# Optimization experiments

Measured on AMD Instinct MI355X. Metric: run time of the kernel, lower is better.

## Reference

```python
import jax, jax.numpy as jnp
import numpy as np

B, NF, S, L, H, MID, KS, NC, DENSE = 16, 8, 16, 256, 128, 32, 8, 10, 512
COEFF = 0.1
BN_EPS = 1e-5


def _normalize(x):
    return x / jnp.maximum(jnp.linalg.norm(x, axis=-1, keepdims=True), 1e-12)


def _sparsemax(z):
    # sparsemax over last axis (Martins & Astudillo 2016)
    zs = jnp.flip(jnp.sort(z, axis=-1), axis=-1)
    k = jnp.arange(1, z.shape[-1] + 1, dtype=z.dtype)
    cum = jnp.cumsum(zs, axis=-1)
    support = (1.0 + k * zs) > cum
    ksup = jnp.sum(support, axis=-1, keepdims=True)
    tau = (jnp.take_along_axis(cum, ksup - 1, axis=-1) - 1.0) / ksup.astype(z.dtype)
    return jnp.maximum(z - tau, 0.0)


def _bn_ncl(x, g, b, m, v):  # eval-mode BatchNorm1d on [N, C, L]
    return g[None, :, None] * (x - m[None, :, None]) * jax.lax.rsqrt(v[None, :, None] + BN_EPS) + b[None, :, None]


def _bn_nc(x, g, b, m, v):  # eval-mode BatchNorm1d on [N, C]
    return g * (x - m) * jax.lax.rsqrt(v + BN_EPS) + b


def _conv(x, w, pad):
    return jax.lax.conv_general_dilated(x, w, (1,), [(pad, pad)], dimension_numbers=('NCH', 'OIH', 'NCH'))


def _maxpool2(x):  # MaxPool1d(kernel=2, stride=2, padding=1): -inf padded
    return jax.lax.reduce_window(x, -jnp.inf, jax.lax.max, (1, 1, 2), (1, 1, 2), ((0, 0), (0, 0), (1, 1)))


def _cnn(x, cw1, bn1, cw2, bn2, cw3, bn3):
    x = _maxpool2(jax.nn.relu(_bn_ncl(_conv(x, cw1, KS // 2), *bn1)))
    x = _maxpool2(jax.nn.relu(_bn_ncl(_conv(x, cw2, 4), *bn2)))
    x = _maxpool2(jax.nn.relu(_bn_ncl(_conv(x, cw3, 4), *bn3)))
    return jnp.mean(x, axis=-1)  # AdaptiveAvgPool1d(1) -> [N, H]


def _alpha_beta(x, cw1, bn1, cw2, bn2, cw3, bn3, Wq, bq, Wk, bk, Wv, bv):
    b = x.shape[0]
    xf = jnp.transpose(x, (1, 0, 2, 3)).reshape(NF, b * S, 1, L)
    rep = jax.vmap(_cnn)(xf, cw1, bn1, cw2, bn2, cw3, bn3)  # [F, B*S, H]
    rep = rep.reshape(NF, b, S, H)
    Q = jax.nn.elu(rep @ Wq + bq)
    K = jax.nn.leaky_relu(rep @ Wk + bk)
    V = jax.nn.leaky_relu(rep @ Wv + bv)
    # mean_t(Q @ K^T) == Q @ mean_t(K); then scale by sqrt(d_k)
    scores = jnp.einsum('fbsh,fbh->fbs', Q, jnp.mean(K, axis=2)) / jnp.sqrt(jnp.float32(H))
    intra_aw = _sparsemax(scores)                             # [F, B, S]
    Z = _normalize(jnp.einsum('fbs,fbsh->fbh', intra_aw, V))  # [F, B, H]
    Kn = _normalize(rep)
    inter_scores = jnp.einsum('ibh,fbsh->ifbs', Z, Kn)        # cosine scores (Z already unit-norm)
    inter_aw = _sparsemax(inter_scores)                       # [I, F, B, S]
    U = jnp.einsum('ifbs,fbsh->ibh', inter_aw, rep) / NF      # mean over feature axis f
    Hc = _normalize(jnp.concatenate([Z, U], axis=-1))         # [F, B, 2H]
    feat = jnp.transpose(Hc, (1, 0, 2)).reshape(b, NF * 2 * H)
    return feat, intra_aw, inter_aw


def _forward(src_x, src_y, tgt_x, cw1, bn1_g, bn1_b, bn1_m, bn1_v, cw2, bn2_g, bn2_b, bn2_m, bn2_v, cw3, bn3_g, bn3_b, bn3_m, bn3_v, Wq, bq, Wk, bk, Wv, bv, bnc1_g, bnc1_b, bnc1_m, bnc1_v, W1, b1, bnc2_g, bnc2_b, bnc2_m, bnc2_v, W2, b2):
    bn1 = (bn1_g, bn1_b, bn1_m, bn1_v)
    bn2 = (bn2_g, bn2_b, bn2_m, bn2_v)
    bn3 = (bn3_g, bn3_b, bn3_m, bn3_v)
    sf, sa, sb = _alpha_beta(src_x, cw1, bn1, cw2, bn2, cw3, bn3, Wq, bq, Wk, bk, Wv, bv)
    _, ta, tb = _alpha_beta(tgt_x, cw1, bn1, cw2, bn2, cw3, bn3, Wq, bq, Wk, bk, Wv, bv)
    h = _bn_nc(sf, bnc1_g, bnc1_b, bnc1_m, bnc1_v) @ W1 + b1
    h = jax.nn.leaky_relu(_bn_nc(h, bnc2_g, bnc2_b, bnc2_m, bnc2_v))
    y_pred = jax.nn.softmax(h @ W2 + b2, axis=-1)
    # MMD domain losses (detached in original via torch.tensor(list))
    da = jnp.mean(sa - ta, axis=-2)                           # [F, S]
    loss_a = COEFF * jnp.mean(jnp.linalg.norm(da, axis=-1))
    db = jnp.mean(sb - tb, axis=-2)                           # [I, F, S]
    loss_b = COEFF * jnp.mean(jnp.sqrt(jnp.sum(db * db, axis=(1, 2))))
    dom = jax.lax.stop_gradient(loss_a + loss_b)
    # CrossEntropyLoss applied to already-softmaxed preds, as in source
    logp = jax.nn.log_softmax(y_pred, axis=-1)
    ce = -jnp.mean(logp[jnp.arange(y_pred.shape[0]), src_y])
    return y_pred, ce + dom


def setup_inputs() -> dict:
    ks = jax.random.split(jax.random.key(0), 40)
    rn = lambda i, sh, s=1.0: s * jax.random.normal(ks[i], sh, dtype=jnp.float32)
    ru = lambda i, sh, lo, hi: jax.random.uniform(ks[i], sh, jnp.float32, lo, hi)
    return {
        'src_x': rn(0, (B, NF, S, L)),
        'src_y': jax.random.randint(ks[1], (B,), 0, NC),
        'tgt_x': rn(2, (B, NF, S, L)),
        'cw1': rn(3, (NF, MID, 1, KS), 0.1),
        'bn1_g': ru(4, (NF, MID), 0.75, 1.25), 'bn1_b': rn(5, (NF, MID), 0.1),
        'bn1_m': rn(6, (NF, MID), 0.1), 'bn1_v': ru(7, (NF, MID), 0.5, 1.5),
        'cw2': rn(8, (NF, 2 * MID, MID, 8), 0.05),
        'bn2_g': ru(9, (NF, 2 * MID), 0.75, 1.25), 'bn2_b': rn(10, (NF, 2 * MID), 0.1),
        'bn2_m': rn(11, (NF, 2 * MID), 0.1), 'bn2_v': ru(12, (NF, 2 * MID), 0.5, 1.5),
        'cw3': rn(13, (NF, H, 2 * MID, 8), 0.05),
        'bn3_g': ru(14, (NF, H), 0.75, 1.25), 'bn3_b': rn(15, (NF, H), 0.1),
        'bn3_m': rn(16, (NF, H), 0.1), 'bn3_v': ru(17, (NF, H), 0.5, 1.5),
        'Wq': rn(18, (H, H), 0.05), 'bq': rn(19, (H,), 0.02),
        'Wk': rn(20, (H, H), 0.05), 'bk': rn(21, (H,), 0.02),
        'Wv': rn(22, (H, H), 0.05), 'bv': rn(23, (H,), 0.02),
        'bnc1_g': ru(24, (NF * 2 * H,), 0.75, 1.25), 'bnc1_b': rn(25, (NF * 2 * H,), 0.1),
        'bnc1_m': rn(26, (NF * 2 * H,), 0.1), 'bnc1_v': ru(27, (NF * 2 * H,), 0.5, 1.5),
        'W1': rn(28, (NF * 2 * H, DENSE), 0.03), 'b1': rn(29, (DENSE,), 0.02),
        'bnc2_g': ru(30, (DENSE,), 0.75, 1.25), 'bnc2_b': rn(31, (DENSE,), 0.1),
        'bnc2_m': rn(32, (DENSE,), 0.1), 'bnc2_v': ru(33, (DENSE,), 0.5, 1.5),
        'W2': rn(34, (DENSE, NC), 0.05), 'b2': rn(35, (NC,), 0.02),
    }


def reference(src_x, src_y, tgt_x, cw1, bn1_g, bn1_b, bn1_m, bn1_v, cw2, bn2_g, bn2_b, bn2_m, bn2_v, cw3, bn3_g, bn3_b, bn3_m, bn3_v, Wq, bq, Wk, bk, Wv, bv, bnc1_g, bnc1_b, bnc1_m, bnc1_v, W1, b1, bnc2_g, bnc2_b, bnc2_m, bnc2_v, W2, b2):
    return _forward(src_x, src_y, tgt_x, cw1, bn1_g, bn1_b, bn1_m, bn1_v, cw2, bn2_g, bn2_b, bn2_m, bn2_v, cw3, bn3_g, bn3_b, bn3_m, bn3_v, Wq, bq, Wk, bk, Wv, bv, bnc1_g, bnc1_b, bnc1_m, bnc1_v, W1, b1, bnc2_g, bnc2_b, bnc2_m, bnc2_v, W2, b2)
```

## Files before the change

### kernel.cpp

```cpp
#include <hip/hip_runtime.h>

typedef unsigned short u16;
typedef unsigned int u32;
typedef __attribute__((ext_vector_type(8))) short bfrag;
typedef __attribute__((ext_vector_type(4))) float ffrag;
typedef __attribute__((ext_vector_type(16))) float ffrag16;

__device__ __forceinline__ float lrelu(float x) { return x >= 0.f ? x : 0.01f * x; }
__device__ __forceinline__ float eluf(float x)  { return x > 0.f ? x : expm1f(x); }
__device__ __forceinline__ u16 f2bf(float f) {
    u32 x = __float_as_uint(f);
    return (u16)((x + 0x7fffu + ((x >> 16) & 1u)) >> 16);
}
__device__ __forceinline__ u16 f2bt(float f) {
    return (u16)(__float_as_uint(f) >> 16);
}
__device__ __forceinline__ float bf2f(u16 u) {
    return __uint_as_float(((u32)u) << 16);
}

__device__ void sparsemax16(const float* z, float* out) {
    float zs[16];
    for (int i = 0; i < 16; ++i) zs[i] = z[i];
    for (int i = 1; i < 16; ++i) {
        float key = zs[i]; int j = i - 1;
        while (j >= 0 && zs[j] < key) { zs[j + 1] = zs[j]; --j; }
        zs[j + 1] = key;
    }
    float cum[16];
    cum[0] = zs[0];
    for (int i = 1; i < 16; ++i) cum[i] = cum[i - 1] + zs[i];
    int ksup = 0;
    for (int k = 1; k <= 16; ++k)
        if (1.0f + (float)k * zs[k - 1] > cum[k - 1]) ksup++;
    if (ksup < 1) ksup = 1;
    float tau = (cum[ksup - 1] - 1.0f) / (float)ksup;
    for (int i = 0; i < 16; ++i) out[i] = fmaxf(z[i] - tau, 0.0f);
}

__global__ __launch_bounds__(256) void k_wprep(
    const float* __restrict__ w2, const float* __restrict__ w3,
    const float* __restrict__ Wq, const float* __restrict__ Wk,
    const float* __restrict__ Wv,
    u16* __restrict__ wpk2, u16* __restrict__ wpk3, u16* __restrict__ wqkv)
{
    int s0 = (blockIdx.x * 256 + threadIdx.x) * 4;
    if (s0 < 131072) {
        float4 v = *reinterpret_cast<const float4*>(w2 + s0);
        float vv[4] = {v.x, v.y, v.z, v.w};
#pragma unroll
        for (int t = 0; t < 4; ++t) {
            int s = s0 + t;
            int kc = s & 7, ci = (s >> 3) & 31, co = (s >> 8) & 63, f = s >> 14;
            int L = ((ci >> 3) << 4) | (co & 15);
            wpk2[f * 16384 + (co >> 4) * 4096 + kc * 512 + L * 8 + (ci & 7)] = f2bf(vv[t]);
        }
    } else if (s0 < 131072 + 524288) {
        int s0b = s0 - 131072;
        float4 v = *reinterpret_cast<const float4*>(w3 + s0b);
        float vv[4] = {v.x, v.y, v.z, v.w};
#pragma unroll
        for (int t = 0; t < 4; ++t) {
            int s = s0b + t;
            int tap = s & 7, ci = (s >> 3) & 63, co = (s >> 9) & 127, f = s >> 16;
            int kt = tap * 4 + (ci >> 4);
            int L = (((ci >> 3) & 1) << 5) | (co & 31);
            wpk3[f * 65536 + (co >> 5) * 16384 + kt * 512 + L * 8 + (ci & 7)] = f2bf(vv[t]);
        }
    } else if (s0 < 131072 + 524288 + 49152) {
        int s0c = s0 - 655360;
        int proj = s0c >> 14, sidx0 = s0c & 16383;
        const float* W = proj == 0 ? Wq : (proj == 1 ? Wk : Wv);
        float4 v = *reinterpret_cast<const float4*>(W + sidx0);
        float vv[4] = {v.x, v.y, v.z, v.w};
#pragma unroll
        for (int t = 0; t < 4; ++t) {
            int s = sidx0 + t;
            int n = s & 127, k = s >> 7;
            int r = k & 31;
            int L = ((r >> 3) << 4) | (n & 15);
            wqkv[proj * 16384 + (n >> 4) * 2048 + (k >> 5) * 512 + L * 8 + (r & 7)] = f2bf(vv[t]);
        }
    }
}

#define S1T_STRIDE 40
#define S2T_STRIDE 72
#define RB2_STRIDE 68
#define RB3_STRIDE 140
#define RB_OFF 6336
#define SMEM_U16 (RB_OFF + 67 * RB3_STRIDE)

__global__ __launch_bounds__(256, 3) void k_cnn(
    const float* __restrict__ xs, const float* __restrict__ xt,
    const float* __restrict__ w1, const float* __restrict__ g1, const float* __restrict__ b1,
    const float* __restrict__ m1, const float* __restrict__ v1,
    const float* __restrict__ g2, const float* __restrict__ b2,
    const float* __restrict__ m2, const float* __restrict__ v2,
    const float* __restrict__ g3, const float* __restrict__ b3,
    const float* __restrict__ m3, const float* __restrict__ v3,
    const u16* __restrict__ wpk2, const u16* __restrict__ wpk3,
    float* __restrict__ rep)
{
    __shared__ __align__(16) u16 smem[SMEM_U16];
    float* xin = (float*)(smem + RB_OFF);

    int tid = threadIdx.x, blk = blockIdx.x;
    int pass = blk >> 11, f = (blk >> 8) & 7, n = blk & 255;
    int bb = n >> 4, ss = n & 15;
    int lane = tid & 63, w = tid >> 6;
    const float* x = pass ? xt : xs;
    float* rep_p = rep + (size_t)pass * 262144;

    {
        u32* z = (u32*)smem;
        for (int i = tid; i < 80; i += 256) z[i] = 0;
        for (int i = tid; i < 360; i += 256) z[2660 + i] = 0;
        if (tid < 4) { xin[tid] = 0.f; xin[260 + tid] = 0.f; }
        const float* xr = x + (((size_t)bb * 8 + f) * 16 + ss) * 256;
        for (int i = tid; i < 256; i += 256) xin[i + 4] = xr[i];
    }
    __syncthreads();

    if (tid < 208) {
        int cc = tid & 7, jc = tid >> 3;
        int co0 = cc * 4, j0 = jc * 5;
        float wr[4][8];
        for (int c = 0; c < 4; ++c) {
            const float4* q = reinterpret_cast<const float4*>(w1 + ((size_t)f * 32 + co0 + c) * 8);
            float4 a = q[0], bq = q[1];
            wr[c][0] = a.x; wr[c][1] = a.y; wr[c][2] = a.z; wr[c][3] = a.w;
            wr[c][4] = bq.x; wr[c][5] = bq.y; wr[c][6] = bq.z; wr[c][7] = bq.w;
        }
        int px[10];
        for (int i = 0; i < 10; ++i) {
            int p = 2 * j0 - 1 + i;
            px[i] = p < 0 ? 0 : (p > 256 ? 256 : p);
        }
        float acc[4][10];
        for (int c = 0; c < 4; ++c) for (int i = 0; i < 10; ++i) acc[c][i] = 0.f;
        for (int k = 0; k < 8; ++k) {
            float xv[10];
            for (int i = 0; i < 10; ++i) xv[i] = xin[px[i] + k];
            for (int c = 0; c < 4; ++c)
                for (int i = 0; i < 10; ++i) acc[c][i] += wr[c][k] * xv[i];
        }
        float scv[4], shv[4];
        for (int c = 0; c < 4; ++c) {
            int co = co0 + c;
            scv[c] = g1[f * 32 + co] * rsqrtf(v1[f * 32 + co] + 1e-5f);
            shv[c] = b1[f * 32 + co] - m1[f * 32 + co] * scv[c];
        }
        for (int jj = 0; jj < 5; ++jj) {
            int j = j0 + jj;
            if (j < 129) {
                ushort4 pk;
                {
                    float a0 = fmaxf(acc[0][2*jj] * scv[0] + shv[0], 0.f);
                    float a1 = fmaxf(acc[0][2*jj+1] * scv[0] + shv[0], 0.f);
                    pk.x = f2bt(fmaxf(a0, a1));
                }
                {
                    float a0 = fmaxf(acc[1][2*jj] * scv[1] + shv[1], 0.f);
                    float a1 = fmaxf(acc[1][2*jj+1] * scv[1] + shv[1], 0.f);
                    pk.y = f2bt(fmaxf(a0, a1));
                }
                {
                    float a0 = fmaxf(acc[2][2*jj] * scv[2] + shv[2], 0.f);
                    float a1 = fmaxf(acc[2][2*jj+1] * scv[2] + shv[2], 0.f);
                    pk.z = f2bt(fmaxf(a0, a1));
                }
                {
                    float a0 = fmaxf(acc[3][2*jj] * scv[3] + shv[3], 0.f);
                    float a1 = fmaxf(acc[3][2*jj+1] * scv[3] + shv[3], 0.f);
                    pk.w = f2bt(fmaxf(a0, a1));
                }
                *reinterpret_cast<ushort4*>(&smem[(j + 4) * S1T_STRIDE + co0]) = pk;
            }
        }
    }
    __syncthreads();

    {
        bfrag B2[2][8];
        {
            const bfrag* gB = reinterpret_cast<const bfrag*>(wpk2);
            int wN = w & 1;
#pragma unroll
            for (int t = 0; t < 2; ++t)
#pragma unroll
                for (int kc = 0; kc < 8; ++kc)
                    B2[t][kc] = gB[(((size_t)f * 4 + (wN * 2 + t)) * 8 + kc) * 64 + lane];
        }
        int wM = w >> 1, wN = w & 1;
        float sc2[2], sh2[2];
        int co2[2];
#pragma unroll
        for (int t = 0; t < 2; ++t) {
            int co = (wN * 2 + t) * 16 + (lane & 15);
            co2[t] = co;
            sc2[t] = g2[f * 64 + co] * rsqrtf(v2[f * 64 + co] + 1e-5f);
            sh2[t] = b2[f * 64 + co] - m2[f * 64 + co] * sc2[t];
        }
        int arow = lane & 15, ci0 = (lane >> 4) << 3;
        int mtlo = wM ? 5 : 0, mthi = wM ? 9 : 5;
        for (int mt = mtlo; mt < mthi; ++mt) {
            ffrag C0 = {0.f, 0.f, 0.f, 0.f}, C1 = {0.f, 0.f, 0.f, 0.f};
            int rb = mt * 16 + arow;
#pragma unroll
            for (int kc = 0; kc < 8; ++kc) {
                bfrag A = *reinterpret_cast<const bfrag*>(&smem[(rb + kc) * S1T_STRIDE + ci0]);
                C0 = __builtin_amdgcn_mfma_f32_16x16x32_bf16(A, B2[0][kc], C0, 0, 0, 0);
                C1 = __builtin_amdgcn_mfma_f32_16x16x32_bf16(A, B2[1][kc], C1, 0, 0, 0);
            }
            int p0 = mt * 16 + ((lane >> 4) << 2);
#pragma unroll
            for (int r = 0; r < 4; ++r) {
                int p = p0 + r;
                if (p < 130) {
                    smem[RB_OFF + p * RB2_STRIDE + co2[0]] = f2bt(fmaxf(C0[r] * sc2[0] + sh2[0], 0.f));
                    smem[RB_OFF + p * RB2_STRIDE + co2[1]] = f2bt(fmaxf(C1[r] * sc2[1] + sh2[1], 0.f));
                }
            }
        }
    }
    __syncthreads();

    {
        u32* z = (u32*)smem;
        for (int i = tid; i < 144; i += 256) z[i] = 0;
        for (int i = tid; i < 612; i += 256) z[2520 + i] = 0;
    }
    {
        const u32* rb2 = reinterpret_cast<const u32*>(smem + RB_OFF);
        u32* s2 = reinterpret_cast<u32*>(smem);
        for (int e = tid; e < 66 * 32; e += 256) {
            int j = e >> 5, c2 = e & 31;
            u32 v;
            if (j == 0) {
                v = rb2[c2];
            } else if (j == 65) {
                v = rb2[129 * 34 + c2];
            } else {
                u32 a = rb2[(2 * j - 1) * 34 + c2];
                u32 b = rb2[(2 * j) * 34 + c2];
                float a0 = bf2f((u16)a), a1 = bf2f((u16)(a >> 16));
                float b0 = bf2f((u16)b), b1 = bf2f((u16)(b >> 16));
                u16 m0 = a0 > b0 ? (u16)a : (u16)b;
                u16 m1 = a1 > b1 ? (u16)(a >> 16) : (u16)(b >> 16);
                v = (u32)m0 | ((u32)m1 << 16);
            }
            s2[(j + 4) * 36 + c2] = v;
        }
    }
    __syncthreads();

    {
        int am = lane & 31, hk = (lane >> 5) << 3;
        const bfrag* gB3 = reinterpret_cast<const bfrag*>(wpk3);
        size_t bbase = (((size_t)f * 4 + w) * 32) * 64 + lane;
        ffrag16 C0 = {0.f,0.f,0.f,0.f,0.f,0.f,0.f,0.f,0.f,0.f,0.f,0.f,0.f,0.f,0.f,0.f};
        ffrag16 C1 = {0.f,0.f,0.f,0.f,0.f,0.f,0.f,0.f,0.f,0.f,0.f,0.f,0.f,0.f,0.f,0.f};
        ffrag16 C2 = {0.f,0.f,0.f,0.f,0.f,0.f,0.f,0.f,0.f,0.f,0.f,0.f,0.f,0.f,0.f,0.f};
#pragma unroll 4
        for (int kt = 0; kt < 32; ++kt) {
            int row0 = am + (kt >> 2);
            int ci0 = (kt & 3) * 16 + hk;
            bfrag B = gB3[bbase + (size_t)kt * 64];
            bfrag A0 = *reinterpret_cast<const bfrag*>(&smem[row0 * S2T_STRIDE + ci0]);
            bfrag A1 = *reinterpret_cast<const bfrag*>(&smem[(row0 + 32) * S2T_STRIDE + ci0]);
            bfrag A2 = *reinterpret_cast<const bfrag*>(&smem[(row0 + 64) * S2T_STRIDE + ci0]);
            C0 = __builtin_amdgcn_mfma_f32_32x32x16_bf16(A0, B, C0, 0, 0, 0);
            C1 = __builtin_amdgcn_mfma_f32_32x32x16_bf16(A1, B, C1, 0, 0, 0);
            C2 = __builtin_amdgcn_mfma_f32_32x32x16_bf16(A2, B, C2, 0, 0, 0);
        }
        int ncol = w * 32 + am;
        float sc = g3[f * 128 + ncol] * rsqrtf(v3[f * 128 + ncol] + 1e-5f);
        float sh = b3[f * 128 + ncol] - m3[f * 128 + ncol] * sc;
        int prow_off = (lane >> 5) << 2;
#pragma unroll
        for (int reg = 0; reg < 16; ++reg) {
            int pr = (reg & 3) + 8 * (reg >> 2) + prow_off;
            smem[RB_OFF + pr * RB3_STRIDE + ncol] = f2bt(fmaxf(C0[reg] * sc + sh, 0.f));
            smem[RB_OFF + (32 + pr) * RB3_STRIDE + ncol] = f2bt(fmaxf(C1[reg] * sc + sh, 0.f));
            int p2 = 64 + pr;
            if (p2 < 67)
                smem[RB_OFF + p2 * RB3_STRIDE + ncol] = f2bt(fmaxf(C2[reg] * sc + sh, 0.f));
        }
    }
    __syncthreads();

    if (tid < 128) {
        int co = tid;
        float sum = bf2f(smem[RB_OFF + 0 * RB3_STRIDE + co]);
        for (int j = 1; j < 34; ++j) {
            float a0 = bf2f(smem[RB_OFF + (2 * j - 1) * RB3_STRIDE + co]);
            float a1 = bf2f(smem[RB_OFF + (2 * j) * RB3_STRIDE + co]);
            sum += fmaxf(a0, a1);
        }
        rep_p[(((size_t)f * 256) + n) * 128 + co] = sum * (1.0f / 34.0f);
    }
}

__global__ __launch_bounds__(256) void k_attn1(
    const float* __restrict__ rep, const u16* __restrict__ wqkv,
    const float* __restrict__ bq, const float* __restrict__ bk,
    const float* __restrict__ bv,
    float* __restrict__ Zn, float* __restrict__ rninv, float* __restrict__ iaw)
{
    __shared__ __align__(16) u16 repbf[16 * 136];
    __shared__ float KmL[128], ZL[128], awL[16], scoresL[16], r2L[16];
    __shared__ float spart[4][4][4];
    __shared__ float redL[4];
    int tid = threadIdx.x;
    int pass = blockIdx.x >> 7, f = (blockIdx.x >> 4) & 7, b = blockIdx.x & 15;
    const float* rp = rep + (size_t)pass * 262144 + ((size_t)f * 256 + b * 16) * 128;
    float* Zn_p = Zn + (size_t)pass * 16384;
    float* rninv_p = rninv + (size_t)pass * 2048;
    float* iaw_p = iaw + (size_t)pass * 2048;

    {
        int s = tid >> 4, i = tid & 15, h0 = i * 8;
        const float4* q4 = reinterpret_cast<const float4*>(rp + s * 128 + h0);
        float4 a = q4[0], c = q4[1];
        float p2 = a.x*a.x + a.y*a.y + a.z*a.z + a.w*a.w
                 + c.x*c.x + c.y*c.y + c.z*c.z + c.w*c.w;
        bfrag pk;
        pk[0] = (short)f2bt(a.x); pk[1] = (short)f2bt(a.y);
        pk[2] = (short)f2bt(a.z); pk[3] = (short)f2bt(a.w);
        pk[4] = (short)f2bt(c.x); pk[5] = (short)f2bt(c.y);
        pk[6] = (short)f2bt(c.z); pk[7] = (short)f2bt(c.w);
        *reinterpret_cast<bfrag*>(&repbf[s * 136 + h0]) = pk;
        p2 += __shfl_xor(p2, 1); p2 += __shfl_xor(p2, 2);
        p2 += __shfl_xor(p2, 4); p2 += __shfl_xor(p2, 8);
        if (i == 0) r2L[s] = p2;
    }
    __syncthreads();

    int lane = tid & 63, w = tid >> 6, arow = lane & 15, q = lane >> 4;
    bfrag A[4];
    for (int kc = 0; kc < 4; ++kc)
        A[kc] = *reinterpret_cast<const bfrag*>(&repbf[arow * 136 + kc * 32 + q * 8]);

    float qv[2][4], vvv[2][4];
    int colv[2];
    const bfrag* BB = reinterpret_cast<const bfrag*>(wqkv);
    for (int t = 0; t < 2; ++t) {
        int nt = w * 2 + t;
        ffrag cq = {0.f,0.f,0.f,0.f}, ck = {0.f,0.f,0.f,0.f}, cv = {0.f,0.f,0.f,0.f};
        for (int kc = 0; kc < 4; ++kc) {
            int fi = (nt * 4 + kc) * 64 + lane;
            bfrag Bq = BB[fi];
            bfrag Bk = BB[2048 + fi];
            bfrag Bv = BB[4096 + fi];
            cq = __builtin_amdgcn_mfma_f32_16x16x32_bf16(A[kc], Bq, cq, 0, 0, 0);
            ck = __builtin_amdgcn_mfma_f32_16x16x32_bf16(A[kc], Bk, ck, 0, 0, 0);
            cv = __builtin_amdgcn_mfma_f32_16x16x32_bf16(A[kc], Bv, cv, 0, 0, 0);
        }
        int col = nt * 16 + arow;
        colv[t] = col;
        float bqc = bq[col], bkc = bk[col], bvc = bv[col];
        float kpt = 0.f;
        for (int r = 0; r < 4; ++r) {
            qv[t][r] = eluf(cq[r] + bqc);
            vvv[t][r] = lrelu(cv[r] + bvc);
            kpt += lrelu(ck[r] + bkc);
        }
        kpt += __shfl_xor(kpt, 16);
        kpt += __shfl_xor(kpt, 32);
        if (q == 0) KmL[col] = kpt * (1.f / 16.f);
    }
    __syncthreads();

    {
        float km0 = KmL[colv[0]], km1 = KmL[colv[1]];
        float ps[4];
        for (int r = 0; r < 4; ++r) {
            float v = qv[0][r] * km0 + qv[1][r] * km1;
            v += __shfl_xor(v, 1); v += __shfl_xor(v, 2);
            v += __shfl_xor(v, 4); v += __shfl_xor(v, 8);
            ps[r] = v;
        }
        if (arow == 0)
            for (int r = 0; r < 4; ++r) spart[w][q][r] = ps[r];
    }
    __syncthreads();
    if (tid < 16) {
        int qq = tid >> 2, rr = tid & 3;
        float sc = spart[0][qq][rr] + spart[1][qq][rr] + spart[2][qq][rr] + spart[3][qq][rr];
        scoresL[tid] = sc * 0.08838834764831845f;
        rninv_p[f * 256 + b * 16 + tid] = 1.f / fmaxf(sqrtf(r2L[tid]), 1e-12f);
    }
    __syncthreads();
    if (tid == 0) sparsemax16(scoresL, awL);
    __syncthreads();
    if (tid < 16) iaw_p[f * 256 + b * 16 + tid] = awL[tid];

    for (int t = 0; t < 2; ++t) {
        float zp = 0.f;
        for (int r = 0; r < 4; ++r) zp += awL[q * 4 + r] * vvv[t][r];
        zp += __shfl_xor(zp, 16);
        zp += __shfl_xor(zp, 32);
        if (q == 0) ZL[colv[t]] = zp;
    }
    __syncthreads();
    if (tid < 128) {
        float z = ZL[tid];
        float v = z * z;
        v += __shfl_xor(v, 1); v += __shfl_xor(v, 2); v += __shfl_xor(v, 4);
        v += __shfl_xor(v, 8); v += __shfl_xor(v, 16); v += __shfl_xor(v, 32);
        if (lane == 0) redL[w] = v;
    }
    __syncthreads();
    if (tid == 0) redL[2] = 1.f / fmaxf(sqrtf(redL[0] + redL[1]), 1e-12f);
    __syncthreads();
    if (tid < 128)
        Zn_p[((size_t)f * 16 + b) * 128 + tid] = ZL[tid] * redL[2];
}

__global__ __launch_bounds__(256) void k_attn2(
    const float* __restrict__ rep, const float* __restrict__ Zn,
    const float* __restrict__ rninv, float* __restrict__ ibw,
    const float* __restrict__ g, const float* __restrict__ bb,
    const float* __restrict__ mm, const float* __restrict__ vv,
    float* __restrict__ featbn)
{
    __shared__ float repL[16384];
    __shared__ float ZiL[128], scores[128], UL[128];
    __shared__ float awLf[8][16];
    __shared__ float redL[2];
    int tid = threadIdx.x, blk = blockIdx.x;
    int pass = blk >> 7, b = (blk >> 3) & 15, i = blk & 7;
    const float* rep_p = rep + (size_t)pass * 262144;

    for (int f = 0; f < 8; ++f) {
        const float4* src = reinterpret_cast<const float4*>(
            rep_p + ((size_t)f * 256 + b * 16) * 128);
        float4* dst = reinterpret_cast<float4*>(repL + f * 2048);
        for (int t = tid; t < 512; t += 256) dst[t] = src[t];
    }
    if (tid < 128) ZiL[tid] = Zn[(size_t)pass * 16384 + ((size_t)i * 16 + b) * 128 + tid];
    __syncthreads();

    if (tid < 128) {
        int f = tid >> 4, s = tid & 15;
        const float* rr = repL + tid * 128;
        float a = 0.f;
        for (int h = 0; h < 128; ++h) a += ZiL[h] * rr[h];
        scores[tid] = a * rninv[(size_t)pass * 2048 + f * 256 + b * 16 + s];
    }
    __syncthreads();
    if (tid < 8) {
        float aw[16];
        sparsemax16(&scores[tid * 16], aw);
        for (int s = 0; s < 16; ++s) awLf[tid][s] = aw[s];
    }
    __syncthreads();
    if (tid < 128) {
        int f = tid >> 4, s = tid & 15;
        ibw[(size_t)pass * 16384 + (((size_t)i * 8 + f) * 16 + b) * 16 + s] = awLf[f][s];
    }
    if (pass == 0) {
        if (tid < 128) {
            int h = tid;
            float u = 0.f;
            for (int f = 0; f < 8; ++f) {
                const float* rr = repL + f * 2048 + h;
                const float* aa = awLf[f];
                for (int s = 0; s < 16; ++s) u += aa[s] * rr[s * 128];
            }
            UL[h] = u * 0.125f;
        }
        __syncthreads();
        if (tid < 128) {
            int lane = tid & 63, w = tid >> 6;
            float v = ZiL[tid] * ZiL[tid] + UL[tid] * UL[tid];
            v += __shfl_xor(v, 1); v += __shfl_xor(v, 2); v += __shfl_xor(v, 4);
            v += __shfl_xor(v, 8); v += __shfl_xor(v, 16); v += __shfl_xor(v, 32);
            if (lane == 0) redL[w] = v;
        }
        __syncthreads();
        if (tid < 256) {
            float inv = 1.f / fmaxf(sqrtf(redL[0] + redL[1]), 1e-12f);
            int d = tid;
            int e = i * 256 + d;
            float val = (d < 128 ? ZiL[d] : UL[d - 128]) * inv;
            float scv = g[e] * rsqrtf(vv[e] + 1e-5f);
            featbn[b * 2048 + e] = (val - mm[e]) * scv + bb[e];
        }
    }
}

__global__ __launch_bounds__(256) void k_head1(
    const float* __restrict__ featbn,
    const float* __restrict__ W1, const float* __restrict__ b1,
    const float* __restrict__ g2, const float* __restrict__ bb2,
    const float* __restrict__ mm2, const float* __restrict__ vv2,
    float* __restrict__ h2ws)
{
    __shared__ float featL[2048];
    __shared__ float part[32][32];
    int tid = threadIdx.x, blk = blockIdx.x;
    int b = blk >> 4, cc = blk & 15;
    {
        const float4* src = reinterpret_cast<const float4*>(featbn + b * 2048);
        float4* dst = reinterpret_cast<float4*>(featL);
        for (int i = tid; i < 512; i += 256) dst[i] = src[i];
    }
    __syncthreads();
    int ks = tid >> 3, cg = tid & 7;
    int col0 = cc * 32 + cg * 4;
    float4 acc = {0.f, 0.f, 0.f, 0.f};
    const float* fl = featL + ks * 64;
    for (int c = 0; c < 64; ++c) {
        int k = ks * 64 + c;
        float4 wv = *reinterpret_cast<const float4*>(W1 + (size_t)k * 512 + col0);
        float fv = fl[c];
        acc.x += fv * wv.x; acc.y += fv * wv.y;
        acc.z += fv * wv.z; acc.w += fv * wv.w;
    }
    part[ks][cg * 4 + 0] = acc.x;
    part[ks][cg * 4 + 1] = acc.y;
    part[ks][cg * 4 + 2] = acc.z;
    part[ks][cg * 4 + 3] = acc.w;
    __syncthreads();
    if (tid < 32) {
        int colw = cc * 32 + tid;
        float s = b1[colw];
        for (int k2 = 0; k2 < 32; ++k2) s += part[k2][tid];
        float scv = g2[colw] * rsqrtf(vv2[colw] + 1e-5f);
        float val = (s - mm2[colw]) * scv + bb2[colw];
        h2ws[b * 512 + colw] = lrelu(val);
    }
}

__global__ __launch_bounds__(256) void k_tail(
    const float* __restrict__ h2ws,
    const float* __restrict__ W2, const float* __restrict__ b2,
    const float* __restrict__ sa, const float* __restrict__ ta,
    const float* __restrict__ sb, const float* __restrict__ tb,
    const int* __restrict__ sy, float* __restrict__ dout)
{
    __shared__ float h2L[8192];
    __shared__ float lgL[160], ypL[160];
    __shared__ float sA[8], sB[8];
    int tid = threadIdx.x;
    for (int i = tid; i < 8192; i += 256) h2L[i] = h2ws[i];
    if (tid < 8) { sA[tid] = 0.f; sB[tid] = 0.f; }
    __syncthreads();
    if (tid < 160) {
        int b = tid / 10, j = tid - b * 10;
        float a = b2[j];
        const float* h = h2L + b * 512;
        for (int c = 0; c < 512; ++c) a += h[c] * W2[c * 10 + j];
        lgL[tid] = a;
    }
    __syncthreads();
    if (tid < 16) {
        int b = tid;
        float mx = lgL[b * 10];
        for (int j = 1; j < 10; ++j) mx = fmaxf(mx, lgL[b * 10 + j]);
        float sum = 0.f, ex[10];
        for (int j = 0; j < 10; ++j) { ex[j] = expf(lgL[b * 10 + j] - mx); sum += ex[j]; }
        for (int j = 0; j < 10; ++j) {
            float p = ex[j] / sum;
            ypL[b * 10 + j] = p;
            dout[b * 10 + j] = p;
        }
    }
    __syncthreads();
    if (tid < 128) {
        int f = tid >> 4, s = tid & 15;
        float d = 0.f;
        for (int b = 0; b < 16; ++b) d += sa[f * 256 + b * 16 + s] - ta[f * 256 + b * 16 + s];
        d *= (1.f / 16.f);
        atomicAdd(&sA[f], d * d);
    }
    for (int e = tid; e < 1024; e += 256) {
        int i = e >> 7, f = (e >> 4) & 7, s = e & 15;
        float d = 0.f;
        int base = ((i * 8 + f) * 16) * 16 + s;
        for (int b = 0; b < 16; ++b) d += sb[base + b * 16] - tb[base + b * 16];
        d *= (1.f / 16.f);
        atomicAdd(&sB[i], d * d);
    }
    __syncthreads();
    if (tid == 0) {
        float la = 0.f, lb = 0.f;
        for (int f = 0; f < 8; ++f) la += sqrtf(sA[f]);
        for (int i = 0; i < 8; ++i) lb += sqrtf(sB[i]);
        la *= 0.1f / 8.f;
        lb *= 0.1f / 8.f;
        float ce = 0.f;
        for (int b = 0; b < 16; ++b) {
            const float* y = ypL + b * 10;
            float mx = y[0];
            for (int j = 1; j < 10; ++j) mx = fmaxf(mx, y[j]);
            float sum = 0.f;
            for (int j = 0; j < 10; ++j) sum += expf(y[j] - mx);
            float lse = mx + logf(sum);
            ce += lse - y[sy[b]];
        }
        ce *= (1.f / 16.f);
        dout[160] = ce + la + lb;
    }
}

extern "C" void kernel_launch(void* const* d_in, const int* in_sizes, int n_in,
                              void* d_out, int out_size, void* d_ws, size_t ws_size,
                              hipStream_t stream) {
    (void)in_sizes; (void)n_in; (void)out_size; (void)ws_size;
    const float* src_x = (const float*)d_in[0];
    const int*   src_y = (const int*)d_in[1];
    const float* tgt_x = (const float*)d_in[2];
    const float *cw1 = (const float*)d_in[3], *bn1g = (const float*)d_in[4],
                *bn1b = (const float*)d_in[5], *bn1m = (const float*)d_in[6],
                *bn1v = (const float*)d_in[7];
    const float *cw2 = (const float*)d_in[8], *bn2g = (const float*)d_in[9],
                *bn2b = (const float*)d_in[10], *bn2m = (const float*)d_in[11],
                *bn2v = (const float*)d_in[12];
    const float *cw3 = (const float*)d_in[13], *bn3g = (const float*)d_in[14],
                *bn3b = (const float*)d_in[15], *bn3m = (const float*)d_in[16],
                *bn3v = (const float*)d_in[17];
    const float *Wq = (const float*)d_in[18], *bq = (const float*)d_in[19],
                *Wk = (const float*)d_in[20], *bk = (const float*)d_in[21],
                *Wv = (const float*)d_in[22], *bv = (const float*)d_in[23];
    const float *bc1g = (const float*)d_in[24], *bc1b = (const float*)d_in[25],
                *bc1m = (const float*)d_in[26], *bc1v = (const float*)d_in[27];
    const float *W1 = (const float*)d_in[28], *b1 = (const float*)d_in[29];
    const float *bc2g = (const float*)d_in[30], *bc2b = (const float*)d_in[31],
                *bc2m = (const float*)d_in[32], *bc2v = (const float*)d_in[33];
    const float *W2 = (const float*)d_in[34], *b2 = (const float*)d_in[35];

    float* ws = (float*)d_ws;
    size_t o = 0;
    float* rep    = ws + o; o += (size_t)2 * 262144;
    float* Zn     = ws + o; o += (size_t)2 * 16384;
    float* rninv  = ws + o; o += (size_t)2 * 2048;
    float* ia     = ws + o; o += (size_t)2 * 2048;
    float* ib     = ws + o; o += (size_t)2 * 16384;
    float* featbn = ws + o; o += (size_t)16 * 2048;
    float* h2ws   = ws + o; o += (size_t)16 * 512;
    u16* wpk2 = (u16*)(ws + o); o += 65536;
    u16* wpk3 = (u16*)(ws + o); o += 262144;
    u16* wqkv = (u16*)(ws + o); o += 24576;

    k_wprep<<<688, 256, 0, stream>>>(cw2, cw3, Wq, Wk, Wv, wpk2, wpk3, wqkv);
    k_cnn<<<4096, 256, 0, stream>>>(src_x, tgt_x,
        cw1, bn1g, bn1b, bn1m, bn1v,
        bn2g, bn2b, bn2m, bn2v,
        bn3g, bn3b, bn3m, bn3v,
        wpk2, wpk3, rep);
    k_attn1<<<256, 256, 0, stream>>>(rep, wqkv, bq, bk, bv, Zn, rninv, ia);
    k_attn2<<<256, 256, 0, stream>>>(rep, Zn, rninv, ib, bc1g, bc1b, bc1m, bc1v, featbn);
    k_head1<<<256, 256, 0, stream>>>(featbn, W1, b1, bc2g, bc2b, bc2m, bc2v, h2ws);
    k_tail<<<1, 256, 0, stream>>>(h2ws, W2, b2, ia, ia + 2048, ib, ib + 16384,
                                  src_y, (float*)d_out);
}
```

Baseline: 298.6 us.

## Fuse attention, cross-attention and dense head into one per-batch kernel

Merges k_attn1, k_attn2 and k_head1 into a single k_mid kernel with one block per (pass, batch) pair, 32 blocks in total. Each block loops over the features and keeps Zn, rninv and the batch-normed features in shared memory. This removes two kernel launches and the Zn, rninv and featbn round trips through global memory. In exchange, the grid drops from 256 blocks to 32, and each pass-0 block streams the whole W1 matrix serially, which leaves most CUs idle and makes the work latency-bound.

New measurement: 597.1 us. +100.0%, slower.

```diff
diff --git a/kernel.cpp b/kernel.cpp
--- a/kernel.cpp
+++ b/kernel.cpp
@@ -302,235 +302,220 @@
     }
 }
 
-__global__ __launch_bounds__(256) void k_attn1(
+__global__ __launch_bounds__(256) void k_mid(
     const float* __restrict__ rep, const u16* __restrict__ wqkv,
     const float* __restrict__ bq, const float* __restrict__ bk,
     const float* __restrict__ bv,
-    float* __restrict__ Zn, float* __restrict__ rninv, float* __restrict__ iaw)
+    float* __restrict__ ia, float* __restrict__ ib,
+    const float* __restrict__ c1g, const float* __restrict__ c1b,
+    const float* __restrict__ c1m, const float* __restrict__ c1v,
+    const float* __restrict__ W1, const float* __restrict__ b1,
+    const float* __restrict__ c2g, const float* __restrict__ c2b,
+    const float* __restrict__ c2m, const float* __restrict__ c2v,
+    float* __restrict__ h2ws)
 {
     __shared__ __align__(16) u16 repbf[16 * 136];
     __shared__ float KmL[128], ZL[128], awL[16], scoresL[16], r2L[16];
     __shared__ float spart[4][4][4];
     __shared__ float redL[4];
-    int tid = threadIdx.x;
-    int pass = blockIdx.x >> 7, f = (blockIdx.x >> 4) & 7, b = blockIdx.x & 15;
-    const float* rp = rep + (size_t)pass * 262144 + ((size_t)f * 256 + b * 16) * 128;
-    float* Zn_p = Zn + (size_t)pass * 16384;
-    float* rninv_p = rninv + (size_t)pass * 2048;
-    float* iaw_p = iaw + (size_t)pass * 2048;
-
-    {
-        int s = tid >> 4, i = tid & 15, h0 = i * 8;
-        const float4* q4 = reinterpret_cast<const float4*>(rp + s * 128 + h0);
-        float4 a = q4[0], c = q4[1];
-        float p2 = a.x*a.x + a.y*a.y + a.z*a.z + a.w*a.w
-                 + c.x*c.x + c.y*c.y + c.z*c.z + c.w*c.w;
-        bfrag pk;
-        pk[0] = (short)f2bt(a.x); pk[1] = (short)f2bt(a.y);
-        pk[2] = (short)f2bt(a.z); pk[3] = (short)f2bt(a.w);
-        pk[4] = (short)f2bt(c.x); pk[5] = (short)f2bt(c.y);
-        pk[6] = (short)f2bt(c.z); pk[7] = (short)f2bt(c.w);
-        *reinterpret_cast<bfrag*>(&repbf[s * 136 + h0]) = pk;
-        p2 += __shfl_xor(p2, 1); p2 += __shfl_xor(p2, 2);
-        p2 += __shfl_xor(p2, 4); p2 += __shfl_xor(p2, 8);
-        if (i == 0) r2L[s] = p2;
-    }
-    __syncthreads();
-
-    int lane = tid & 63, w = tid >> 6, arow = lane & 15, q = lane >> 4;
-    bfrag A[4];
-    for (int kc = 0; kc < 4; ++kc)
-        A[kc] = *reinterpret_cast<const bfrag*>(&repbf[arow * 136 + kc * 32 + q * 8]);
-
-    float qv[2][4], vvv[2][4];
-    int colv[2];
-    const bfrag* BB = reinterpret_cast<const bfrag*>(wqkv);
-    for (int t = 0; t < 2; ++t) {
-        int nt = w * 2 + t;
-        ffrag cq = {0.f,0.f,0.f,0.f}, ck = {0.f,0.f,0.f,0.f}, cv = {0.f,0.f,0.f,0.f};
-        for (int kc = 0; kc < 4; ++kc) {
-            int fi = (nt * 4 + kc) * 64 + lane;
-            bfrag Bq = BB[fi];
-            bfrag Bk = BB[2048 + fi];
-            bfrag Bv = BB[4096 + fi];
-            cq = __builtin_amdgcn_mfma_f32_16x16x32_bf16(A[kc], Bq, cq, 0, 0, 0);
-            ck = __builtin_amdgcn_mfma_f32_16x16x32_bf16(A[kc], Bk, ck, 0, 0, 0);
-            cv = __builtin_amdgcn_mfma_f32_16x16x32_bf16(A[kc], Bv, cv, 0, 0, 0);
-        }
-        int col = nt * 16 + arow;
-        colv[t] = col;
-        float bqc = bq[col], bkc = bk[col], bvc = bv[col];
-        float kpt = 0.f;
-        for (int r = 0; r < 4; ++r) {
-            qv[t][r] = eluf(cq[r] + bqc);
-            vvv[t][r] = lrelu(cv[r] + bvc);
-            kpt += lrelu(ck[r] + bkc);
-        }
-        kpt += __shfl_xor(kpt, 16);
-        kpt += __shfl_xor(kpt, 32);
-        if (q == 0) KmL[col] = kpt * (1.f / 16.f);
-    }
-    __syncthreads();
-
-    {
-        float km0 = KmL[colv[0]], km1 = KmL[colv[1]];
-        float ps[4];
-        for (int r = 0; r < 4; ++r) {
-            float v = qv[0][r] * km0 + qv[1][r] * km1;
-            v += __shfl_xor(v, 1); v += __shfl_xor(v, 2);
-            v += __shfl_xor(v, 4); v += __shfl_xor(v, 8);
-            ps[r] = v;
-        }
-        if (arow == 0)
-            for (int r = 0; r < 4; ++r) spart[w][q][r] = ps[r];
-    }
-    __syncthreads();
-    if (tid < 16) {
-        int qq = tid >> 2, rr = tid & 3;
-        float sc = spart[0][qq][rr] + spart[1][qq][rr] + spart[2][qq][rr] + spart[3][qq][rr];
-        scoresL[tid] = sc * 0.08838834764831845f;
-        rninv_p[f * 256 + b * 16 + tid] = 1.f / fmaxf(sqrtf(r2L[tid]), 1e-12f);
-    }
-    __syncthreads();
-    if (tid == 0) sparsemax16(scoresL, awL);
-    __syncthreads();
-    if (tid < 16) iaw_p[f * 256 + b * 16 + tid] = awL[tid];
-
-    for (int t = 0; t < 2; ++t) {
-        float zp = 0.f;
-        for (int r = 0; r < 4; ++r) zp += awL[q * 4 + r] * vvv[t][r];
-        zp += __shfl_xor(zp, 16);
-        zp += __shfl_xor(zp, 32);
-        if (q == 0) ZL[colv[t]] = zp;
-    }
-    __syncthreads();
-    if (tid < 128) {
-        float z = ZL[tid];
-        float v = z * z;
-        v += __shfl_xor(v, 1); v += __shfl_xor(v, 2); v += __shfl_xor(v, 4);
-        v += __shfl_xor(v, 8); v += __shfl_xor(v, 16); v += __shfl_xor(v, 32);
-        if (lane == 0) redL[w] = v;
-    }
-    __syncthreads();
-    if (tid == 0) redL[2] = 1.f / fmaxf(sqrtf(redL[0] + redL[1]), 1e-12f);
-    __syncthreads();
-    if (tid < 128)
-        Zn_p[((size_t)f * 16 + b) * 128 + tid] = ZL[tid] * redL[2];
-}
-
-__global__ __launch_bounds__(256) void k_attn2(
-    const float* __restrict__ rep, const float* __restrict__ Zn,
-    const float* __restrict__ rninv, float* __restrict__ ibw,
-    const float* __restrict__ g, const float* __restrict__ bb,
-    const float* __restrict__ mm, const float* __restrict__ vv,
-    float* __restrict__ featbn)
-{
-    __shared__ float repL[16384];
-    __shared__ float ZiL[128], scores[128], UL[128];
+    __shared__ float ZnL[8][128];
+    __shared__ float rninvL[8][16];
+    __shared__ float scores2[128], UL[128];
     __shared__ float awLf[8][16];
-    __shared__ float redL[2];
+    __shared__ float featL[2048];
+    __shared__ float part[32][32];
+
     int tid = threadIdx.x, blk = blockIdx.x;
-    int pass = blk >> 7, b = (blk >> 3) & 15, i = blk & 7;
+    int pass = blk >> 4, b = blk & 15;
     const float* rep_p = rep + (size_t)pass * 262144;
+    float* ia_p = ia + (size_t)pass * 2048;
+    int lane = tid & 63, w = tid >> 6;
 
     for (int f = 0; f < 8; ++f) {
-        const float4* src = reinterpret_cast<const float4*>(
-            rep_p + ((size_t)f * 256 + b * 16) * 128);
-        float4* dst = reinterpret_cast<float4*>(repL + f * 2048);
-        for (int t = tid; t < 512; t += 256) dst[t] = src[t];
-    }
-    if (tid < 128) ZiL[tid] = Zn[(size_t)pass * 16384 + ((size_t)i * 16 + b) * 128 + tid];
-    __syncthreads();
-
-    if (tid < 128) {
-        int f = tid >> 4, s = tid & 15;
-        const float* rr = repL + tid * 128;
-        float a = 0.f;
-        for (int h = 0; h < 128; ++h) a += ZiL[h] * rr[h];
-        scores[tid] = a * rninv[(size_t)pass * 2048 + f * 256 + b * 16 + s];
-    }
-    __syncthreads();
-    if (tid < 8) {
-        float aw[16];
-        sparsemax16(&scores[tid * 16], aw);
-        for (int s = 0; s < 16; ++s) awLf[tid][s] = aw[s];
-    }
-    __syncthreads();
-    if (tid < 128) {
-        int f = tid >> 4, s = tid & 15;
-        ibw[(size_t)pass * 16384 + (((size_t)i * 8 + f) * 16 + b) * 16 + s] = awLf[f][s];
-    }
-    if (pass == 0) {
+        __syncthreads();
+        const float* rp = rep_p + ((size_t)f * 256 + b * 16) * 128;
+        {
+            int s = tid >> 4, i = tid & 15, h0 = i * 8;
+            const float4* q4 = reinterpret_cast<const float4*>(rp + s * 128 + h0);
+            float4 a = q4[0], c = q4[1];
+            float p2 = a.x*a.x + a.y*a.y + a.z*a.z + a.w*a.w
+                     + c.x*c.x + c.y*c.y + c.z*c.z + c.w*c.w;
+            bfrag pk;
+            pk[0] = (short)f2bt(a.x); pk[1] = (short)f2bt(a.y);
+            pk[2] = (short)f2bt(a.z); pk[3] = (short)f2bt(a.w);
+            pk[4] = (short)f2bt(c.x); pk[5] = (short)f2bt(c.y);
+            pk[6] = (short)f2bt(c.z); pk[7] = (short)f2bt(c.w);
+            *reinterpret_cast<bfrag*>(&repbf[s * 136 + h0]) = pk;
+            p2 += __shfl_xor(p2, 1); p2 += __shfl_xor(p2, 2);
+            p2 += __shfl_xor(p2, 4); p2 += __shfl_xor(p2, 8);
+            if (i == 0) r2L[s] = p2;
+        }
+        __syncthreads();
+
+        int arow = lane & 15, q = lane >> 4;
+        bfrag A[4];
+        for (int kc = 0; kc < 4; ++kc)
+            A[kc] = *reinterpret_cast<const bfrag*>(&repbf[arow * 136 + kc * 32 + q * 8]);
+
+        float qv[2][4], vvv[2][4];
+        int colv[2];
+        const bfrag* BB = reinterpret_cast<const bfrag*>(wqkv);
+        for (int t = 0; t < 2; ++t) {
+            int nt = w * 2 + t;
+            ffrag cq = {0.f,0.f,0.f,0.f}, ck = {0.f,0.f,0.f,0.f}, cv = {0.f,0.f,0.f,0.f};
+            for (int kc = 0; kc < 4; ++kc) {
+                int fi = (nt * 4 + kc) * 64 + lane;
+                bfrag Bq = BB[fi];
+                bfrag Bk = BB[2048 + fi];
+                bfrag Bv = BB[4096 + fi];
+                cq = __builtin_amdgcn_mfma_f32_16x16x32_bf16(A[kc], Bq, cq, 0, 0, 0);
+                ck = __builtin_amdgcn_mfma_f32_16x16x32_bf16(A[kc], Bk, ck, 0, 0, 0);
+                cv = __builtin_amdgcn_mfma_f32_16x16x32_bf16(A[kc], Bv, cv, 0, 0, 0);
+            }
+            int col = nt * 16 + arow;
+            colv[t] = col;
+            float bqc = bq[col], bkc = bk[col], bvc = bv[col];
+            float kpt = 0.f;
+            for (int r = 0; r < 4; ++r) {
+                qv[t][r] = eluf(cq[r] + bqc);
+                vvv[t][r] = lrelu(cv[r] + bvc);
+                kpt += lrelu(ck[r] + bkc);
+            }
+            kpt += __shfl_xor(kpt, 16);
+            kpt += __shfl_xor(kpt, 32);
+            if (q == 0) KmL[col] = kpt * (1.f / 16.f);
+        }
+        __syncthreads();
+
+        {
+            float km0 = KmL[colv[0]], km1 = KmL[colv[1]];
+            float ps[4];
+            for (int r = 0; r < 4; ++r) {
+                float v = qv[0][r] * km0 + qv[1][r] * km1;
+                v += __shfl_xor(v, 1); v += __shfl_xor(v, 2);
+                v += __shfl_xor(v, 4); v += __shfl_xor(v, 8);
+                ps[r] = v;
+            }
+            if (arow == 0)
+                for (int r = 0; r < 4; ++r) spart[w][q][r] = ps[r];
+        }
+        __syncthreads();
+        if (tid < 16) {
+            int qq = tid >> 2, rr = tid & 3;
+            float sc = spart[0][qq][rr] + spart[1][qq][rr] + spart[2][qq][rr] + spart[3][qq][rr];
+            scoresL[tid] = sc * 0.08838834764831845f;
+            rninvL[f][tid] = 1.f / fmaxf(sqrtf(r2L[tid]), 1e-12f);
+        }
+        __syncthreads();
+        if (tid == 0) sparsemax16(scoresL, awL);
+        __syncthreads();
+        if (tid < 16) ia_p[f * 256 + b * 16 + tid] = awL[tid];
+
+        for (int t = 0; t < 2; ++t) {
+            float zp = 0.f;
+            for (int r = 0; r < 4; ++r) zp += awL[q * 4 + r] * vvv[t][r];
+            zp += __shfl_xor(zp, 16);
+            zp += __shfl_xor(zp, 32);
+            if (q == 0) ZL[colv[t]] = zp;
+        }
+        __syncthreads();
         if (tid < 128) {
-            int h = tid;
-            float u = 0.f;
-            for (int f = 0; f < 8; ++f) {
-                const float* rr = repL + f * 2048 + h;
-                const float* aa = awLf[f];
-                for (int s = 0; s < 16; ++s) u += aa[s] * rr[s * 128];
-            }
-            UL[h] = u * 0.125f;
-        }
-        __syncthreads();
-        if (tid < 128) {
-            int lane = tid & 63, w = tid >> 6;
-            float v = ZiL[tid] * ZiL[tid] + UL[tid] * UL[tid];
+            float z = ZL[tid];
+            float v = z * z;
             v += __shfl_xor(v, 1); v += __shfl_xor(v, 2); v += __shfl_xor(v, 4);
             v += __shfl_xor(v, 8); v += __shfl_xor(v, 16); v += __shfl_xor(v, 32);
             if (lane == 0) redL[w] = v;
         }
         __syncthreads();
-        if (tid < 256) {
-            float inv = 1.f / fmaxf(sqrtf(redL[0] + redL[1]), 1e-12f);
-            int d = tid;
-            int e = i * 256 + d;
-            float val = (d < 128 ? ZiL[d] : UL[d - 128]) * inv;
-            float scv = g[e] * rsqrtf(vv[e] + 1e-5f);
-            featbn[b * 2048 + e] = (val - mm[e]) * scv + bb[e];
-        }
-    }
-}
-
-__global__ __launch_bounds__(256) void k_head1(
-    const float* __restrict__ featbn,
-    const float* __restrict__ W1, const float* __restrict__ b1,
-    const float* __restrict__ g2, const float* __restrict__ bb2,
-    const float* __restrict__ mm2, const float* __restrict__ vv2,
-    float* __restrict__ h2ws)
-{
-    __shared__ float featL[2048];
-    __shared__ float part[32][32];
-    int tid = threadIdx.x, blk = blockIdx.x;
-    int b = blk >> 4, cc = blk & 15;
-    {
-        const float4* src = reinterpret_cast<const float4*>(featbn + b * 2048);
-        float4* dst = reinterpret_cast<float4*>(featL);
-        for (int i = tid; i < 512; i += 256) dst[i] = src[i];
-    }
-    __syncthreads();
-    int ks = tid >> 3, cg = tid & 7;
-    int col0 = cc * 32 + cg * 4;
-    float4 acc = {0.f, 0.f, 0.f, 0.f};
-    const float* fl = featL + ks * 64;
-    for (int c = 0; c < 64; ++c) {
-        int k = ks * 64 + c;
-        float4 wv = *reinterpret_cast<const float4*>(W1 + (size_t)k * 512 + col0);
-        float fv = fl[c];
-        acc.x += fv * wv.x; acc.y += fv * wv.y;
-        acc.z += fv * wv.z; acc.w += fv * wv.w;
-    }
-    part[ks][cg * 4 + 0] = acc.x;
-    part[ks][cg * 4 + 1] = acc.y;
-    part[ks][cg * 4 + 2] = acc.z;
-    part[ks][cg * 4 + 3] = acc.w;
-    __syncthreads();
-    if (tid < 32) {
-        int colw = cc * 32 + tid;
-        float s = b1[colw];
-        for (int k2 = 0; k2 < 32; ++k2) s += part[k2][tid];
-        float scv = g2[colw] * rsqrtf(vv2[colw] + 1e-5f);
-        float val = (s - mm2[colw]) * scv + bb2[colw];
-        h2ws[b * 512 + colw] = lrelu(val);
+        if (tid == 0) redL[2] = 1.f / fmaxf(sqrtf(redL[0] + redL[1]), 1e-12f);
+        __syncthreads();
+        if (tid < 128)
+            ZnL[f][tid] = ZL[tid] * redL[2];
+    }
+    __syncthreads();
+
+    for (int i = 0; i < 8; ++i) {
+        const float* ZiL = ZnL[i];
+        if (tid < 128) {
+            int f = tid >> 4, s = tid & 15;
+            const float* rr = rep_p + ((size_t)f * 256 + b * 16 + s) * 128;
+            float a = 0.f;
+            for (int h = 0; h < 128; h += 4) {
+                float4 q = *reinterpret_cast<const float4*>(rr + h);
+                a += ZiL[h] * q.x + ZiL[h + 1] * q.y + ZiL[h + 2] * q.z + ZiL[h + 3] * q.w;
+            }
+            scores2[tid] = a * rninvL[f][s];
+        }
+        __syncthreads();
+        if (tid < 8) {
+            float aw[16];
+            sparsemax16(&scores2[tid * 16], aw);
+            for (int s = 0; s < 16; ++s) awLf[tid][s] = aw[s];
+        }
+        __syncthreads();
+        if (tid < 128) {
+            int f = tid >> 4, s = tid & 15;
+            ib[(size_t)pass * 16384 + (((size_t)i * 8 + f) * 16 + b) * 16 + s] = awLf[f][s];
+        }
+        if (pass == 0) {
+            if (tid < 128) {
+                int h = tid;
+                float u = 0.f;
+                for (int f = 0; f < 8; ++f) {
+                    const float* rr = rep_p + ((size_t)f * 256 + b * 16) * 128 + h;
+                    const float* aa = awLf[f];
+                    for (int s = 0; s < 16; ++s) u += aa[s] * rr[s * 128];
+                }
+                UL[h] = u * 0.125f;
+            }
+            __syncthreads();
+            if (tid < 128) {
+                float v = ZiL[tid] * ZiL[tid] + UL[tid] * UL[tid];
+                v += __shfl_xor(v, 1); v += __shfl_xor(v, 2); v += __shfl_xor(v, 4);
+                v += __shfl_xor(v, 8); v += __shfl_xor(v, 16); v += __shfl_xor(v, 32);
+                if (lane == 0) redL[w] = v;
+            }
+            __syncthreads();
+            {
+                float inv = 1.f / fmaxf(sqrtf(redL[0] + redL[1]), 1e-12f);
+                int d = tid;
+                int e = i * 256 + d;
+                float val = (d < 128 ? ZiL[d] : UL[d - 128]) * inv;
+                float scv = c1g[e] * rsqrtf(c1v[e] + 1e-5f);
+                featL[e] = (val - c1m[e]) * scv + c1b[e];
+            }
+        }
+        __syncthreads();
+    }
+
+    if (pass == 0) {
+        for (int cc = 0; cc < 16; ++cc) {
+            int ks = tid >> 3, cg2 = tid & 7;
+            int col0 = cc * 32 + cg2 * 4;
+            float4 acc = {0.f, 0.f, 0.f, 0.f};
+            const float* fl = featL + ks * 64;
+            for (int c = 0; c < 64; ++c) {
+                int k = ks * 64 + c;
+                float4 wv = *reinterpret_cast<const float4*>(W1 + (size_t)k * 512 + col0);
+                float fv = fl[c];
+                acc.x += fv * wv.x; acc.y += fv * wv.y;
+                acc.z += fv * wv.z; acc.w += fv * wv.w;
+            }
+            part[ks][cg2 * 4 + 0] = acc.x;
+            part[ks][cg2 * 4 + 1] = acc.y;
+            part[ks][cg2 * 4 + 2] = acc.z;
+            part[ks][cg2 * 4 + 3] = acc.w;
+            __syncthreads();
+            if (tid < 32) {
+                int colw = cc * 32 + tid;
+                float s = b1[colw];
+                for (int k2 = 0; k2 < 32; ++k2) s += part[k2][tid];
+                float scv = c2g[colw] * rsqrtf(c2v[colw] + 1e-5f);
+                float val = (s - c2m[colw]) * scv + c2b[colw];
+                h2ws[b * 512 + colw] = lrelu(val);
+            }
+            __syncthreads();
+        }
     }
 }
 
@@ -635,11 +620,8 @@
     float* ws = (float*)d_ws;
     size_t o = 0;
     float* rep    = ws + o; o += (size_t)2 * 262144;
-    float* Zn     = ws + o; o += (size_t)2 * 16384;
-    float* rninv  = ws + o; o += (size_t)2 * 2048;
     float* ia     = ws + o; o += (size_t)2 * 2048;
     float* ib     = ws + o; o += (size_t)2 * 16384;
-    float* featbn = ws + o; o += (size_t)16 * 2048;
     float* h2ws   = ws + o; o += (size_t)16 * 512;
     u16* wpk2 = (u16*)(ws + o); o += 65536;
     u16* wpk3 = (u16*)(ws + o); o += 262144;
@@ -651,9 +633,8 @@
         bn2g, bn2b, bn2m, bn2v,
         bn3g, bn3b, bn3m, bn3v,
         wpk2, wpk3, rep);
-    k_attn1<<<256, 256, 0, stream>>>(rep, wqkv, bq, bk, bv, Zn, rninv, ia);
-    k_attn2<<<256, 256, 0, stream>>>(rep, Zn, rninv, ib, bc1g, bc1b, bc1m, bc1v, featbn);
-    k_head1<<<256, 256, 0, stream>>>(featbn, W1, b1, bc2g, bc2b, bc2m, bc2v, h2ws);
+    k_mid<<<32, 256, 0, stream>>>(rep, wqkv, bq, bk, bv, ia, ib,
+        bc1g, bc1b, bc1m, bc1v, W1, b1, bc2g, bc2b, bc2m, bc2v, h2ws);
     k_tail<<<1, 256, 0, stream>>>(h2ws, W2, b2, ia, ia + 2048, ib, ib + 16384,
                                   src_y, (float*)d_out);
 }
```
